# Optimization experiments

Hardware: AMD Instinct MI355X
Metric: run time of the kernel (lower is better)

Reference implementation:

```python
import jax, jax.numpy as jnp
import numpy as np

KERNEL_NUM = 21
SIGMA = 0.1
EXACT_SIGMA = 0.001
EPS = 1e-8  # torch F.cosine_similarity eps


def _kernel_params():
    n = KERNEL_NUM - 1
    mus = [1.0 / n + 2.0 * i / n - 1.0 for i in range(n)] + [1.0]
    sigmas = [SIGMA] * n + [EXACT_SIGMA]
    return jnp.asarray(mus, jnp.float32), jnp.asarray(sigmas, jnp.float32)


def setup_inputs() -> dict:
    key = jax.random.key(0)
    ks = jax.random.split(key, 12)
    B, QL, DL, V, D = 512, 32, 256, 100000, 256
    return {
        "query_1": jax.random.randint(ks[0], (B, QL), 0, V),
        "document_1": jax.random.randint(ks[1], (B, DL), 0, V),
        "query_2": jax.random.randint(ks[2], (B, QL), 0, V),
        "document_2": jax.random.randint(ks[3], (B, DL), 0, V),
        "emb_weight": jax.random.normal(ks[4], (V, D), jnp.float32),
        "W0": jax.random.normal(ks[5], (10, 21), jnp.float32) * 0.2,
        "b0": jax.random.normal(ks[6], (10,), jnp.float32) * 0.1,
        "W1": jax.random.normal(ks[7], (5, 10), jnp.float32) * 0.3,
        "b1": jax.random.normal(ks[8], (5,), jnp.float32) * 0.1,
        "W2": jax.random.normal(ks[9], (1, 5), jnp.float32) * 0.4,
        "b2": jax.random.normal(ks[10], (1,), jnp.float32) * 0.1,
    }


def _predict(query, doc, emb_weight, W0, b0, W1, b1, W2, b2):
    q = emb_weight[query]  # [B, QL, D]
    d = emb_weight[doc]    # [B, DL, D]
    qn = q / jnp.maximum(jnp.linalg.norm(q, axis=-1, keepdims=True), EPS)
    dn = d / jnp.maximum(jnp.linalg.norm(d, axis=-1, keepdims=True), EPS)
    mm = jnp.einsum('bqe,bde->bqd', qn, dn)  # cosine matching matrix [B,QL,DL]
    mus, sigmas = _kernel_params()
    # Gaussian soft binning: [B,QL,DL,K]
    K = jnp.exp(-0.5 * (mm[..., None] - mus) ** 2 / sigmas ** 2)
    km = jnp.log1p(K.sum(axis=2)).sum(axis=1)  # [B, K]
    h = jax.nn.relu(km @ W0.T + b0)
    h = jax.nn.relu(h @ W1.T + b1)
    return h @ W2.T + b2  # [B, 1]


def reference(query_1, document_1, query_2, document_2,
              emb_weight, W0, b0, W1, b1, W2, b2):
    l1 = _predict(query_1, document_1, emb_weight, W0, b0, W1, b1, W2, b2)
    l2 = _predict(query_2, document_2, emb_weight, W0, b0, W1, b1, W2, b2)
    return jax.nn.sigmoid(l1 - l2)
```

## Files before the change

kernel.cpp:

```cpp
#include <hip/hip_runtime.h>
#include <math.h>

typedef __bf16 bf16x8 __attribute__((ext_vector_type(8)));
typedef __bf16 bf16x4 __attribute__((ext_vector_type(4)));
typedef float  f32x4  __attribute__((ext_vector_type(4)));

#define QL    32
#define DL    256
#define DIM   256
#define NK    21
#define KSOFT 20
#define STR   264
#define L2E   1.4426950408889634f

#if __has_builtin(__builtin_amdgcn_exp2f)
#define EXP2F(x) __builtin_amdgcn_exp2f(x)
#else
#define EXP2F(x) exp2f(x)
#endif

__global__ __launch_bounds__(256)
void knrm_prep(const float* __restrict__ emb, __bf16* __restrict__ tab, int V)
{
    const int wave = threadIdx.x >> 6;
    const int lane = threadIdx.x & 63;
    const int row0 = (blockIdx.x * 4 + wave) * 2;
    if (row0 >= V) return;

    float4 a = reinterpret_cast<const float4*>(emb + (size_t)row0 * DIM)[lane];
    float4 c = reinterpret_cast<const float4*>(emb + (size_t)(row0 + 1) * DIM)[lane];
    float sa = a.x*a.x + a.y*a.y + a.z*a.z + a.w*a.w;
    float sc = c.x*c.x + c.y*c.y + c.z*c.z + c.w*c.w;
    #pragma unroll
    for (int m = 32; m; m >>= 1) { sa += __shfl_xor(sa, m); sc += __shfl_xor(sc, m); }
    float ia = rsqrtf(fmaxf(sa, 1e-16f));
    float ic = rsqrtf(fmaxf(sc, 1e-16f));
    bf16x4 oa, oc;
    oa[0] = (__bf16)(a.x * ia); oa[1] = (__bf16)(a.y * ia);
    oa[2] = (__bf16)(a.z * ia); oa[3] = (__bf16)(a.w * ia);
    oc[0] = (__bf16)(c.x * ic); oc[1] = (__bf16)(c.y * ic);
    oc[2] = (__bf16)(c.z * ic); oc[3] = (__bf16)(c.w * ic);
    *reinterpret_cast<bf16x4*>(tab + (size_t)row0 * DIM + lane * 4) = oa;
    *reinterpret_cast<bf16x4*>(tab + (size_t)(row0 + 1) * DIM + lane * 4) = oc;
}

__global__ __launch_bounds__(256, 4)
void knrm_main5(const int* __restrict__ q1t, const int* __restrict__ d1t,
                const int* __restrict__ q2t, const int* __restrict__ d2t,
                const __bf16* __restrict__ tab,
                const float* __restrict__ W0, const float* __restrict__ b0,
                const float* __restrict__ W1, const float* __restrict__ b1,
                const float* __restrict__ W2, const float* __restrict__ b2,
                float* __restrict__ lg, int B)
{
    const int b    = blockIdx.x;
    const int pair = blockIdx.y;
    const int tid  = threadIdx.x;
    const int wave = tid >> 6;
    const int lane = tid & 63;
    const int qt   = wave >> 1;
    const int dt   = wave & 1;
    const int g    = lane >> 4;
    const int cl   = lane & 15;
    const int hl   = lane & 31;
    const int hw   = lane >> 5;

    const int* qtok = pair ? q2t : q1t;
    const int* dtok = pair ? d2t : d1t;

    __shared__ __align__(16) __bf16 qbuf[QL * STR];
    __shared__ __align__(16) __bf16 dbuf[32 * STR];
    __shared__ float Sqk[QL * NK];
    __shared__ int   dtok_s[DL];
    __shared__ int   qtok_s[QL];
    __shared__ float km[NK];
    __shared__ float h0[10];
    __shared__ float h1[5];

    if (tid < QL) qtok_s[tid] = qtok[b * QL + tid];
    dtok_s[tid] = dtok[b * DL + tid];
    for (int e = tid; e < QL * NK; e += 256) Sqk[e] = 0.0f;
    if (tid < NK) km[tid] = 0.0f;
    __syncthreads();

    {
        bf16x8 qv[4];
        #pragma unroll
        for (int i = 0; i < 4; ++i) {
            int r = wave * 8 + i * 2 + hw;
            qv[i] = *reinterpret_cast<const bf16x8*>(
                tab + (size_t)qtok_s[r] * DIM + hl * 8);
        }
        #pragma unroll
        for (int i = 0; i < 4; ++i) {
            int r = wave * 8 + i * 2 + hw;
            *reinterpret_cast<bf16x8*>(&qbuf[r * STR + hl * 8]) = qv[i];
        }
    }

    bf16x8 dreg[4];
    #pragma unroll
    for (int i = 0; i < 4; ++i) {
        int r = wave * 8 + i * 2 + hw;
        dreg[i] = *reinterpret_cast<const bf16x8*>(
            tab + (size_t)dtok_s[r] * DIM + hl * 8);
    }

    const int myq  = qt * 16 + cl;
    const int qtk1 = qtok_s[myq];

    float acc[NK];
    #pragma unroll
    for (int k = 0; k < NK; ++k) acc[k] = 0.0f;

    for (int tile = 0; tile < 8; ++tile) {
        __syncthreads();

        #pragma unroll
        for (int i = 0; i < 4; ++i) {
            int r = wave * 8 + i * 2 + hw;
            *reinterpret_cast<bf16x8*>(&dbuf[r * STR + hl * 8]) = dreg[i];
        }
        if (tile < 7) {
            #pragma unroll
            for (int i = 0; i < 4; ++i) {
                int r = wave * 8 + i * 2 + hw;
                dreg[i] = *reinterpret_cast<const bf16x8*>(
                    tab + (size_t)dtok_s[(tile + 1) * 32 + r] * DIM + hl * 8);
            }
        }
        __syncthreads();

        f32x4 cf = {0.0f, 0.0f, 0.0f, 0.0f};
        #pragma unroll
        for (int ks = 0; ks < 8; ++ks) {
            bf16x8 dfr = *reinterpret_cast<const bf16x8*>(&dbuf[(dt*16 + cl)*STR + ks*32 + g*8]);
            bf16x8 qfr = *reinterpret_cast<const bf16x8*>(&qbuf[(qt*16 + cl)*STR + ks*32 + g*8]);
            cf = __builtin_amdgcn_mfma_f32_16x16x32_bf16(dfr, qfr, cf, 0, 0, 0);
        }

        #pragma unroll
        for (int i = 0; i < 4; ++i) {
            float mm  = cf[i];
            float mm2 = mm * mm;
            #pragma unroll
            for (int k = 0; k < KSOFT; ++k) {
                float mu = -0.95f + 0.1f * (float)k;
                float a1 = 100.0f * L2E * mu;
                float a0 = -50.0f * L2E * mu * mu;
                float arg = fmaf(a1, mm, fmaf(-50.0f * L2E, mm2, a0));
                acc[k] += EXP2F(arg);
            }
            int drow = tile*32 + dt*16 + g*4 + i;
            acc[KSOFT] += (dtok_s[drow] == qtk1) ? 1.0f : 0.0f;
        }
    }

    #pragma unroll
    for (int k = 0; k < NK; ++k)
        atomicAdd(&Sqk[myq * NK + k], acc[k]);
    __syncthreads();

    for (int e = tid; e < QL * NK; e += 256)
        atomicAdd(&km[e % NK], log1pf(Sqk[e]));
    __syncthreads();

    if (tid < 10) {
        float h = b0[tid];
        #pragma unroll
        for (int k = 0; k < NK; ++k) h = fmaf(km[k], W0[tid*NK + k], h);
        h0[tid] = fmaxf(h, 0.0f);
    }
    __syncthreads();
    if (tid < 5) {
        float h = b1[tid];
        #pragma unroll
        for (int j = 0; j < 10; ++j) h = fmaf(h0[j], W1[tid*10 + j], h);
        h1[tid] = fmaxf(h, 0.0f);
    }
    __syncthreads();
    if (tid == 0) {
        float l = b2[0];
        #pragma unroll
        for (int j = 0; j < 5; ++j) l = fmaf(h1[j], W2[j], l);
        lg[pair * B + b] = l;
    }
}

__global__ void knrm_final(const float* __restrict__ lg, float* __restrict__ out, int B)
{
    int i = blockIdx.x * 256 + threadIdx.x;
    if (i < B) {
        float z = lg[i] - lg[B + i];
        out[i] = 1.0f / (1.0f + expf(-z));
    }
}

__global__ __launch_bounds__(256, 2)
void knrm_mono(const int* __restrict__ q1t, const int* __restrict__ d1t,
               const int* __restrict__ q2t, const int* __restrict__ d2t,
               const float* __restrict__ emb,
               const float* __restrict__ W0, const float* __restrict__ b0,
               const float* __restrict__ W1, const float* __restrict__ b1,
               const float* __restrict__ W2, const float* __restrict__ b2,
               float* __restrict__ out)
{
    const int b    = blockIdx.x;
    const int tid  = threadIdx.x;
    const int wave = tid >> 6;
    const int lane = tid & 63;
    const int qt   = wave >> 1;
    const int dt   = wave & 1;
    const int g    = lane >> 4;
    const int cl   = lane & 15;

    __shared__ __align__(16) __bf16 qbuf[QL * STR];
    __shared__ __align__(16) __bf16 dbuf[32 * STR];
    __shared__ float Sqk[QL * NK];
    __shared__ int   dtok_s[DL];
    __shared__ int   qtok_s[QL];
    __shared__ float km[NK];
    __shared__ float h0[10];
    __shared__ float h1[5];
    __shared__ float logit[2];

    for (int pair = 0; pair < 2; ++pair) {
        const int* qtok = pair ? q2t : q1t;
        const int* dtok = pair ? d2t : d1t;

        if (tid < QL) qtok_s[tid] = qtok[b * QL + tid];
        dtok_s[tid] = dtok[b * DL + tid];
        for (int e = tid; e < QL * NK; e += 256) Sqk[e] = 0.0f;
        if (tid < NK) km[tid] = 0.0f;
        __syncthreads();

        #pragma unroll
        for (int i = 0; i < 8; ++i) {
            int row = wave * 8 + i;
            int tok = qtok_s[row];
            float4 v = reinterpret_cast<const float4*>(emb + (size_t)tok * DIM)[lane];
            float s = v.x*v.x + v.y*v.y + v.z*v.z + v.w*v.w;
            #pragma unroll
            for (int m = 32; m; m >>= 1) s += __shfl_xor(s, m);
            float inv = rsqrtf(fmaxf(s, 1e-16f));
            bf16x4 o;
            o[0] = (__bf16)(v.x * inv); o[1] = (__bf16)(v.y * inv);
            o[2] = (__bf16)(v.z * inv); o[3] = (__bf16)(v.w * inv);
            *reinterpret_cast<bf16x4*>(&qbuf[row * STR + lane * 4]) = o;
        }

        int qtk[4];
        #pragma unroll
        for (int i = 0; i < 4; ++i) qtk[i] = qtok_s[qt * 16 + g * 4 + i];

        float acc[4 * NK];
        #pragma unroll
        for (int e = 0; e < 4 * NK; ++e) acc[e] = 0.0f;

        for (int tile = 0; tile < 8; ++tile) {
            #pragma unroll
            for (int i = 0; i < 8; ++i) {
                int r = wave * 8 + i;
                int tok = dtok_s[tile * 32 + r];
                float4 v = reinterpret_cast<const float4*>(emb + (size_t)tok * DIM)[lane];
                float s = v.x*v.x + v.y*v.y + v.z*v.z + v.w*v.w;
                #pragma unroll
                for (int m = 32; m; m >>= 1) s += __shfl_xor(s, m);
                float inv = rsqrtf(fmaxf(s, 1e-16f));
                bf16x4 o;
                o[0] = (__bf16)(v.x * inv); o[1] = (__bf16)(v.y * inv);
                o[2] = (__bf16)(v.z * inv); o[3] = (__bf16)(v.w * inv);
                *reinterpret_cast<bf16x4*>(&dbuf[r * STR + lane * 4]) = o;
            }
            __syncthreads();

            f32x4 cf = {0.0f, 0.0f, 0.0f, 0.0f};
            #pragma unroll
            for (int ks = 0; ks < 8; ++ks) {
                bf16x8 af  = *reinterpret_cast<const bf16x8*>(&qbuf[(qt*16 + cl)*STR + ks*32 + g*8]);
                bf16x8 bfr = *reinterpret_cast<const bf16x8*>(&dbuf[(dt*16 + cl)*STR + ks*32 + g*8]);
                cf = __builtin_amdgcn_mfma_f32_16x16x32_bf16(af, bfr, cf, 0, 0, 0);
            }

            int dtk = dtok_s[tile*32 + dt*16 + cl];
            #pragma unroll
            for (int i = 0; i < 4; ++i) {
                float mm  = cf[i];
                float mm2 = mm * mm;
                #pragma unroll
                for (int k = 0; k < KSOFT; ++k) {
                    float mu = -0.95f + 0.1f * (float)k;
                    float a1 = 100.0f * L2E * mu;
                    float a0 = -50.0f * L2E * mu * mu;
                    float arg = fmaf(a1, mm, fmaf(-50.0f * L2E, mm2, a0));
                    acc[i*NK + k] += EXP2F(arg);
                }
                acc[i*NK + KSOFT] += (dtk == qtk[i]) ? 1.0f : 0.0f;
            }
            __syncthreads();
        }

        #pragma unroll
        for (int i = 0; i < 4; ++i) {
            int row = qt*16 + g*4 + i;
            #pragma unroll
            for (int k = 0; k < NK; ++k)
                atomicAdd(&Sqk[row*NK + k], acc[i*NK + k]);
        }
        __syncthreads();

        for (int e = tid; e < QL * NK; e += 256)
            atomicAdd(&km[e % NK], log1pf(Sqk[e]));
        __syncthreads();

        if (tid < 10) {
            float h = b0[tid];
            #pragma unroll
            for (int k = 0; k < NK; ++k) h = fmaf(km[k], W0[tid*NK + k], h);
            h0[tid] = fmaxf(h, 0.0f);
        }
        __syncthreads();
        if (tid < 5) {
            float h = b1[tid];
            #pragma unroll
            for (int j = 0; j < 10; ++j) h = fmaf(h0[j], W1[tid*10 + j], h);
            h1[tid] = fmaxf(h, 0.0f);
        }
        __syncthreads();
        if (tid == 0) {
            float l = b2[0];
            #pragma unroll
            for (int j = 0; j < 5; ++j) l = fmaf(h1[j], W2[j], l);
            logit[pair] = l;
        }
        __syncthreads();
    }

    if (tid == 0) {
        float z = logit[0] - logit[1];
        out[b] = 1.0f / (1.0f + expf(-z));
    }
}

extern "C" void kernel_launch(void* const* d_in, const int* in_sizes, int n_in,
                              void* d_out, int out_size, void* d_ws, size_t ws_size,
                              hipStream_t stream) {
    const int*   q1  = (const int*)d_in[0];
    const int*   d1  = (const int*)d_in[1];
    const int*   q2  = (const int*)d_in[2];
    const int*   d2  = (const int*)d_in[3];
    const float* emb = (const float*)d_in[4];
    const float* W0  = (const float*)d_in[5];
    const float* b0  = (const float*)d_in[6];
    const float* W1  = (const float*)d_in[7];
    const float* b1  = (const float*)d_in[8];
    const float* W2  = (const float*)d_in[9];
    const float* b2  = (const float*)d_in[10];
    float* out = (float*)d_out;

    const int B = in_sizes[0] / QL;
    const int V = in_sizes[4] / DIM;

    size_t tab_bytes = (size_t)V * DIM * sizeof(__bf16);
    size_t need = tab_bytes + 256 + (size_t)2 * B * sizeof(float);

    if (ws_size >= need) {
        __bf16* tab = (__bf16*)d_ws;
        float*  lg  = (float*)((char*)d_ws + ((tab_bytes + 255) & ~(size_t)255));

        knrm_prep<<<(V/2 + 3) / 4, 256, 0, stream>>>(emb, tab, V);
        dim3 grid(B, 2);
        knrm_main5<<<grid, 256, 0, stream>>>(q1, d1, q2, d2, tab,
                                             W0, b0, W1, b1, W2, b2, lg, B);
        knrm_final<<<(B + 255) / 256, 256, 0, stream>>>(lg, out, B);
    } else {
        knrm_mono<<<B, 256, 0, stream>>>(q1, d1, q2, d2, emb,
                                         W0, b0, W1, b1, W2, b2, out);
    }
}
```

Measured before the change: 238.1 us.

## Load MFMA operands straight from global into registers, dropping LDS staging

The main kernel no longer stages query and document embedding tiles in shared memory. Each lane now loads its MFMA fragments directly from the bf16 table into registers, and the next document tile is prefetched while the current tile is computed. This removes the LDS writes and reads and the two barriers per tile. The cost is redundant global loads, since each query and document row is now fetched by multiple waves, and higher register pressure from holding 16 bf16x8 fragments per lane.

```diff
diff --git a/kernel.cpp b/kernel.cpp
--- a/kernel.cpp
+++ b/kernel.cpp
@@ -45,7 +45,7 @@
 }
 
 __global__ __launch_bounds__(256, 4)
-void knrm_main5(const int* __restrict__ q1t, const int* __restrict__ d1t,
+void knrm_main6(const int* __restrict__ q1t, const int* __restrict__ d1t,
                 const int* __restrict__ q2t, const int* __restrict__ d2t,
                 const __bf16* __restrict__ tab,
                 const float* __restrict__ W0, const float* __restrict__ b0,
@@ -62,14 +62,10 @@
     const int dt   = wave & 1;
     const int g    = lane >> 4;
     const int cl   = lane & 15;
-    const int hl   = lane & 31;
-    const int hw   = lane >> 5;
 
     const int* qtok = pair ? q2t : q1t;
     const int* dtok = pair ? d2t : d1t;
 
-    __shared__ __align__(16) __bf16 qbuf[QL * STR];
-    __shared__ __align__(16) __bf16 dbuf[32 * STR];
     __shared__ float Sqk[QL * NK];
     __shared__ int   dtok_s[DL];
     __shared__ int   qtok_s[QL];
@@ -83,60 +79,42 @@
     if (tid < NK) km[tid] = 0.0f;
     __syncthreads();
 
-    {
-        bf16x8 qv[4];
-        #pragma unroll
-        for (int i = 0; i < 4; ++i) {
-            int r = wave * 8 + i * 2 + hw;
-            qv[i] = *reinterpret_cast<const bf16x8*>(
-                tab + (size_t)qtok_s[r] * DIM + hl * 8);
-        }
-        #pragma unroll
-        for (int i = 0; i < 4; ++i) {
-            int r = wave * 8 + i * 2 + hw;
-            *reinterpret_cast<bf16x8*>(&qbuf[r * STR + hl * 8]) = qv[i];
-        }
-    }
-
-    bf16x8 dreg[4];
-    #pragma unroll
-    for (int i = 0; i < 4; ++i) {
-        int r = wave * 8 + i * 2 + hw;
-        dreg[i] = *reinterpret_cast<const bf16x8*>(
-            tab + (size_t)dtok_s[r] * DIM + hl * 8);
-    }
-
     const int myq  = qt * 16 + cl;
     const int qtk1 = qtok_s[myq];
+
+    bf16x8 qreg[8];
+    {
+        const __bf16* qrow = tab + (size_t)qtk1 * DIM + g * 8;
+        #pragma unroll
+        for (int ks = 0; ks < 8; ++ks)
+            qreg[ks] = *reinterpret_cast<const bf16x8*>(qrow + ks * 32);
+    }
+
+    bf16x8 areg[8];
+    {
+        const int tokA = dtok_s[dt * 16 + cl];
+        const __bf16* drow = tab + (size_t)tokA * DIM + g * 8;
+        #pragma unroll
+        for (int ks = 0; ks < 8; ++ks)
+            areg[ks] = *reinterpret_cast<const bf16x8*>(drow + ks * 32);
+    }
 
     float acc[NK];
     #pragma unroll
     for (int k = 0; k < NK; ++k) acc[k] = 0.0f;
 
     for (int tile = 0; tile < 8; ++tile) {
-        __syncthreads();
-
-        #pragma unroll
-        for (int i = 0; i < 4; ++i) {
-            int r = wave * 8 + i * 2 + hw;
-            *reinterpret_cast<bf16x8*>(&dbuf[r * STR + hl * 8]) = dreg[i];
-        }
+        f32x4 cf = {0.0f, 0.0f, 0.0f, 0.0f};
+        #pragma unroll
+        for (int ks = 0; ks < 8; ++ks)
+            cf = __builtin_amdgcn_mfma_f32_16x16x32_bf16(areg[ks], qreg[ks], cf, 0, 0, 0);
+
         if (tile < 7) {
-            #pragma unroll
-            for (int i = 0; i < 4; ++i) {
-                int r = wave * 8 + i * 2 + hw;
-                dreg[i] = *reinterpret_cast<const bf16x8*>(
-                    tab + (size_t)dtok_s[(tile + 1) * 32 + r] * DIM + hl * 8);
-            }
-        }
-        __syncthreads();
-
-        f32x4 cf = {0.0f, 0.0f, 0.0f, 0.0f};
-        #pragma unroll
-        for (int ks = 0; ks < 8; ++ks) {
-            bf16x8 dfr = *reinterpret_cast<const bf16x8*>(&dbuf[(dt*16 + cl)*STR + ks*32 + g*8]);
-            bf16x8 qfr = *reinterpret_cast<const bf16x8*>(&qbuf[(qt*16 + cl)*STR + ks*32 + g*8]);
-            cf = __builtin_amdgcn_mfma_f32_16x16x32_bf16(dfr, qfr, cf, 0, 0, 0);
+            const int tokA = dtok_s[(tile + 1) * 32 + dt * 16 + cl];
+            const __bf16* drow = tab + (size_t)tokA * DIM + g * 8;
+            #pragma unroll
+            for (int ks = 0; ks < 8; ++ks)
+                areg[ks] = *reinterpret_cast<const bf16x8*>(drow + ks * 32);
         }
 
         #pragma unroll
@@ -151,7 +129,7 @@
                 float arg = fmaf(a1, mm, fmaf(-50.0f * L2E, mm2, a0));
                 acc[k] += EXP2F(arg);
             }
-            int drow = tile*32 + dt*16 + g*4 + i;
+            int drow = tile * 32 + dt * 16 + g * 4 + i;
             acc[KSOFT] += (dtok_s[drow] == qtk1) ? 1.0f : 0.0f;
         }
     }
@@ -370,7 +348,7 @@
 
         knrm_prep<<<(V/2 + 3) / 4, 256, 0, stream>>>(emb, tab, V);
         dim3 grid(B, 2);
-        knrm_main5<<<grid, 256, 0, stream>>>(q1, d1, q2, d2, tab,
+        knrm_main6<<<grid, 256, 0, stream>>>(q1, d1, q2, d2, tab,
                                              W0, b0, W1, b1, W2, b2, lg, B);
         knrm_final<<<(B + 255) / 256, 256, 0, stream>>>(lg, out, B);
     } else {
```

After: 273.2 us. 1.15x slower.

## Double-buffer doc tiles in LDS and keep query fragments in registers

Applied to the files above, without the earlier changes.

Query embedding fragments are loaded straight from global memory into registers (eight bf16x8 per lane) instead of being staged through shared memory. The doc tile buffer is double-buffered, so each iteration needs one barrier instead of two, and the next tile's LDS store is placed after the exp-heavy binning work. This is meant to cut LDS traffic and synchronisation stalls. In exchange it uses more registers, which may affect occupancy under the 4-blocks launch bound, and query loads are now strided per lane.

```diff
diff --git a/kernel.cpp b/kernel.cpp
--- a/kernel.cpp
+++ b/kernel.cpp
@@ -45,7 +45,7 @@
 }
 
 __global__ __launch_bounds__(256, 4)
-void knrm_main5(const int* __restrict__ q1t, const int* __restrict__ d1t,
+void knrm_main7(const int* __restrict__ q1t, const int* __restrict__ d1t,
                 const int* __restrict__ q2t, const int* __restrict__ d2t,
                 const __bf16* __restrict__ tab,
                 const float* __restrict__ W0, const float* __restrict__ b0,
@@ -68,8 +68,7 @@
     const int* qtok = pair ? q2t : q1t;
     const int* dtok = pair ? d2t : d1t;
 
-    __shared__ __align__(16) __bf16 qbuf[QL * STR];
-    __shared__ __align__(16) __bf16 dbuf[32 * STR];
+    __shared__ __align__(16) __bf16 dbuf[2][32 * STR];
     __shared__ float Sqk[QL * NK];
     __shared__ int   dtok_s[DL];
     __shared__ int   qtok_s[QL];
@@ -83,19 +82,15 @@
     if (tid < NK) km[tid] = 0.0f;
     __syncthreads();
 
+    const int myq  = qt * 16 + cl;
+    const int qtk1 = qtok_s[myq];
+
+    bf16x8 qreg[8];
     {
-        bf16x8 qv[4];
-        #pragma unroll
-        for (int i = 0; i < 4; ++i) {
-            int r = wave * 8 + i * 2 + hw;
-            qv[i] = *reinterpret_cast<const bf16x8*>(
-                tab + (size_t)qtok_s[r] * DIM + hl * 8);
-        }
-        #pragma unroll
-        for (int i = 0; i < 4; ++i) {
-            int r = wave * 8 + i * 2 + hw;
-            *reinterpret_cast<bf16x8*>(&qbuf[r * STR + hl * 8]) = qv[i];
-        }
+        const __bf16* qrow = tab + (size_t)qtk1 * DIM + g * 8;
+        #pragma unroll
+        for (int ks = 0; ks < 8; ++ks)
+            qreg[ks] = *reinterpret_cast<const bf16x8*>(qrow + ks * 32);
     }
 
     bf16x8 dreg[4];
@@ -105,22 +100,20 @@
         dreg[i] = *reinterpret_cast<const bf16x8*>(
             tab + (size_t)dtok_s[r] * DIM + hl * 8);
     }
-
-    const int myq  = qt * 16 + cl;
-    const int qtk1 = qtok_s[myq];
+    #pragma unroll
+    for (int i = 0; i < 4; ++i) {
+        int r = wave * 8 + i * 2 + hw;
+        *reinterpret_cast<bf16x8*>(&dbuf[0][r * STR + hl * 8]) = dreg[i];
+    }
+    __syncthreads();
 
     float acc[NK];
     #pragma unroll
     for (int k = 0; k < NK; ++k) acc[k] = 0.0f;
 
     for (int tile = 0; tile < 8; ++tile) {
-        __syncthreads();
-
-        #pragma unroll
-        for (int i = 0; i < 4; ++i) {
-            int r = wave * 8 + i * 2 + hw;
-            *reinterpret_cast<bf16x8*>(&dbuf[r * STR + hl * 8]) = dreg[i];
-        }
+        const int cur = tile & 1;
+
         if (tile < 7) {
             #pragma unroll
             for (int i = 0; i < 4; ++i) {
@@ -129,14 +122,13 @@
                     tab + (size_t)dtok_s[(tile + 1) * 32 + r] * DIM + hl * 8);
             }
         }
-        __syncthreads();
 
         f32x4 cf = {0.0f, 0.0f, 0.0f, 0.0f};
         #pragma unroll
         for (int ks = 0; ks < 8; ++ks) {
-            bf16x8 dfr = *reinterpret_cast<const bf16x8*>(&dbuf[(dt*16 + cl)*STR + ks*32 + g*8]);
-            bf16x8 qfr = *reinterpret_cast<const bf16x8*>(&qbuf[(qt*16 + cl)*STR + ks*32 + g*8]);
-            cf = __builtin_amdgcn_mfma_f32_16x16x32_bf16(dfr, qfr, cf, 0, 0, 0);
+            bf16x8 dfr = *reinterpret_cast<const bf16x8*>(
+                &dbuf[cur][(dt*16 + cl)*STR + ks*32 + g*8]);
+            cf = __builtin_amdgcn_mfma_f32_16x16x32_bf16(dfr, qreg[ks], cf, 0, 0, 0);
         }
 
         #pragma unroll
@@ -151,8 +143,17 @@
                 float arg = fmaf(a1, mm, fmaf(-50.0f * L2E, mm2, a0));
                 acc[k] += EXP2F(arg);
             }
-            int drow = tile*32 + dt*16 + g*4 + i;
+            int drow = tile * 32 + dt * 16 + g * 4 + i;
             acc[KSOFT] += (dtok_s[drow] == qtk1) ? 1.0f : 0.0f;
+        }
+
+        if (tile < 7) {
+            #pragma unroll
+            for (int i = 0; i < 4; ++i) {
+                int r = wave * 8 + i * 2 + hw;
+                *reinterpret_cast<bf16x8*>(&dbuf[cur ^ 1][r * STR + hl * 8]) = dreg[i];
+            }
+            __syncthreads();
         }
     }
 
@@ -370,7 +371,7 @@
 
         knrm_prep<<<(V/2 + 3) / 4, 256, 0, stream>>>(emb, tab, V);
         dim3 grid(B, 2);
-        knrm_main5<<<grid, 256, 0, stream>>>(q1, d1, q2, d2, tab,
+        knrm_main7<<<grid, 256, 0, stream>>>(q1, d1, q2, d2, tab,
                                              W0, b0, W1, b1, W2, b2, lg, B);
         knrm_final<<<(B + 255) / 256, 256, 0, stream>>>(lg, out, B);
     } else {
```

Result: slower. 267.6 us (+12.4%).
